# Kernel tuning notes

Hardware: AMD Instinct MI355X
Metric: run time of the kernel (lower is better)

The kernel has to match this reference:

```python
import jax, jax.numpy as jnp
import numpy as np

ROPE_BASE = 10000.0


def rotate_half(x):
    # interleaved rotate: (x0,x1,x2,x3,...) -> (-x1,x0,-x3,x2,...)
    x1 = x[..., ::2]
    x2 = x[..., 1::2]
    return jnp.stack((-x2, x1), axis=-1).reshape(x.shape)


def rope_cos_sin(seq_len, dim, dtype):
    inv_freq = 1.0 / (ROPE_BASE ** (jnp.arange(0, dim, 2, dtype=jnp.float32) / dim))
    pos = jnp.arange(seq_len, dtype=jnp.float32)
    freqs = jnp.outer(pos, inv_freq)              # [S, dim/2]
    emb = jnp.concatenate([freqs, freqs], axis=-1)  # [S, dim]
    return jnp.cos(emb).astype(dtype), jnp.sin(emb).astype(dtype)


def setup_inputs() -> dict:
    key = jax.random.key(0)
    k1, k2, k3, k4 = jax.random.split(key, 4)
    B, S, D = 4, 4096, 256
    scale = 1.0 / np.sqrt(D)
    x = jax.random.normal(k1, (B, S, D), dtype=jnp.float32)
    wq = jax.random.normal(k2, (D, D), dtype=jnp.float32) * scale
    wk = jax.random.normal(k3, (D, D), dtype=jnp.float32) * scale
    wv = jax.random.normal(k4, (D, D), dtype=jnp.float32) * scale
    return {"x": x, "wq": wq, "wk": wk, "wv": wv}


def reference(x, wq, wk, wv):
    D = x.shape[-1]
    S = x.shape[-2]
    # torch Linear: y = x @ W^T
    q = jnp.einsum('bsd,ed->bse', x, wq)
    k = jnp.einsum('bsd,ed->bse', x, wk)
    v = jnp.einsum('bsd,ed->bse', x, wv)
    cos, sin = rope_cos_sin(S, D, x.dtype)  # [S, D]
    q = q * cos + rotate_half(q) * sin
    k = k * cos + rotate_half(k) * sin
    scores = jnp.einsum('bqd,bkd->bqk', q, k) / jnp.sqrt(jnp.asarray(D, x.dtype))
    weights = jax.nn.softmax(scores, axis=-1)
    output = jnp.einsum('bqk,bkd->bqd', weights, v)
    return output, weights
```

## Files before the change

kernel.cpp:

```cpp
#include <hip/hip_runtime.h>
#include <hip/hip_bf16.h>
#include <stdint.h>


#define B_ 4
#define S_ 4096
#define D_ 256
#define NQ 4194304
#define NW 65536
#define NTAB 524288

typedef __attribute__((ext_vector_type(4))) float f32x4;
typedef __attribute__((ext_vector_type(8))) short short8;
typedef __attribute__((ext_vector_type(4))) short short4v;
typedef __attribute__((ext_vector_type(4))) unsigned uint32x4;

__device__ __forceinline__ short f2bf(float f) {
  unsigned u = __builtin_bit_cast(unsigned, f);
  u += 0x7fffu + ((u >> 16) & 1u);
  return (short)(u >> 16);
}
__device__ __forceinline__ float bf2f(short h) {
  unsigned u = ((unsigned)(unsigned short)h) << 16;
  return __builtin_bit_cast(float, u);
}

__device__ __forceinline__ void gload16(const void* g, void* l) {
  __builtin_amdgcn_global_load_lds(
      (const __attribute__((address_space(1))) unsigned*)g,
      (__attribute__((address_space(3))) unsigned*)l, 16, 0, 0);
}

__global__ __launch_bounds__(256) void k0_split(
    const float* __restrict__ wq, const float* __restrict__ wk,
    const float* __restrict__ wv,
    short* __restrict__ wh, short* __restrict__ wl,
    float* __restrict__ ctab) {
  int idx = blockIdx.x * 256 + threadIdx.x;
  if (idx < 3 * NW) {
    int m = idx >> 16;
    int e = idx & (NW - 1);
    const float* w = (m == 0) ? wq : (m == 1) ? wk : wv;
    float v = w[e];
    short hi = f2bf(v);
    wh[idx] = hi;
    wl[idx] = f2bf(v - bf2f(hi));
  } else {
    int t = idx - 3 * NW;
    int s = t >> 7, j = t & 127;
    float invf = __expf(-0.07195578415606394f * (float)j);
    float sn, cs;
    sincosf((float)s * invf, &sn, &cs);
    ctab[2 * t] = cs;
    ctab[2 * t + 1] = sn;
  }
}

__global__ __launch_bounds__(256) void k1_proj(
    const float* __restrict__ x,
    const short* __restrict__ wh, const short* __restrict__ wl,
    const float* __restrict__ ctab,
    short* __restrict__ qh, short* __restrict__ ql,
    short* __restrict__ kh, short* __restrict__ vt) {
  const int m = blockIdx.y;
  const int b = blockIdx.x >> 6;
  const int sbase = (blockIdx.x & 63) << 6;
  const int tid = threadIdx.x;
  const int w = tid >> 6;
  const int lane = tid & 63;
  const int lr = lane & 15;
  const int g = lane >> 4;

  const int srow = sbase + w * 16 + lr;
  const float* xp = x + ((size_t)(b * S_ + srow)) * D_;
  const short* whm = wh + m * NW;
  const short* wlm = wl + m * NW;

  short8 ah[8], al[8];
#pragma unroll
  for (int dc = 0; dc < 8; ++dc) {
    const float* xe = xp + dc * 32 + g * 8;
    f32x4 v0 = *(const f32x4*)(xe);
    f32x4 v1 = *(const f32x4*)(xe + 4);
#pragma unroll
    for (int j = 0; j < 4; ++j) {
      short h0 = f2bf(v0[j]);
      ah[dc][j] = h0;
      al[dc][j] = f2bf(v0[j] - bf2f(h0));
      short h1 = f2bf(v1[j]);
      ah[dc][4 + j] = h1;
      al[dc][4 + j] = f2bf(v1[j] - bf2f(h1));
    }
  }

  f32x4 acc[16];
#pragma unroll
  for (int i = 0; i < 16; ++i) acc[i] = (f32x4)0.f;

#pragma unroll
  for (int dc = 0; dc < 8; ++dc) {
    const int d = dc * 32 + g * 8;
#pragma unroll
    for (int ct = 0; ct < 16; ++ct) {
      const int e = ct * 16 + lr;
      short8 bh = *(const short8*)(whm + e * D_ + d);
      short8 bl = *(const short8*)(wlm + e * D_ + d);
      acc[ct] = __builtin_amdgcn_mfma_f32_16x16x32_bf16(ah[dc], bh, acc[ct], 0, 0, 0);
      acc[ct] = __builtin_amdgcn_mfma_f32_16x16x32_bf16(ah[dc], bl, acc[ct], 0, 0, 0);
      acc[ct] = __builtin_amdgcn_mfma_f32_16x16x32_bf16(al[dc], bh, acc[ct], 0, 0, 0);
    }
  }

  const int s0 = sbase + w * 16 + g * 4;
  if (m == 2) {
#pragma unroll
    for (int ct = 0; ct < 16; ++ct) {
      const int e = ct * 16 + lr;
      short4v pk;
#pragma unroll
      for (int r = 0; r < 4; ++r) pk[r] = f2bf(acc[ct][r]);
      *(short4v*)(vt + ((size_t)(b * D_ + e)) * S_ + s0) = pk;
    }
  } else {
    short* oh = (m == 0) ? qh : kh;
#pragma unroll
    for (int ct = 0; ct < 16; ++ct) {
      const int e = ct * 16 + lr;
      const float sgn = (e & 1) ? 1.0f : -1.0f;
#pragma unroll
      for (int r = 0; r < 4; ++r) {
        float v = acc[ct][r];
        float p = __shfl_xor(v, 1, 64);
        const float2 cs2 = *(const float2*)(ctab + ((size_t)((s0 + r) << 7) + (e & 127)) * 2);
        float q2 = v * cs2.x + sgn * p * cs2.y;
        short hi = f2bf(q2);
        size_t off = ((size_t)(b * S_ + s0 + r)) * D_ + e;
        oh[off] = hi;
        if (m == 0) ql[off] = f2bf(q2 - bf2f(hi));
      }
    }
  }
}

__global__ __launch_bounds__(256, 3) void k2_fused(
    const short* __restrict__ qh, const short* __restrict__ ql,
    const short* __restrict__ kh, const short* __restrict__ vt,
    float* __restrict__ wts, float* __restrict__ out) {
  __shared__ __align__(16) char kbuf[32768];
  __shared__ __align__(16) char etile[2][2048];
  __shared__ float part[2][32];
  __shared__ float lsum_l[32];

  const int bid = blockIdx.x;
  const int swz = (bid & 7) * 64 + ((bid >> 3) & 31) * 2 + (bid >> 8);
  const int b = swz >> 7;
  const int qbase = (swz & 127) << 5;
  const int tid = threadIdx.x;
  const int w = tid >> 6;
  const int lane = tid & 63;
  const int lr = lane & 15;
  const int g = lane >> 4;
  const int qg = w & 1;
  const int kg = w >> 1;

  short8 qfh[8], qfl[8];
  {
    const int qrow = qbase + qg * 16 + lr;
    const short* ph = qh + ((size_t)(b * S_ + qrow)) * D_;
    const short* pl = ql + ((size_t)(b * S_ + qrow)) * D_;
#pragma unroll
    for (int dc = 0; dc < 8; ++dc) {
      qfh[dc] = *(const short8*)(ph + dc * 32 + g * 8);
      qfl[dc] = *(const short8*)(pl + dc * 32 + g * 8);
    }
  }

  f32x4 acc = (f32x4)0.f;
  f32x4 accv[2][4];
#pragma unroll
  for (int qs = 0; qs < 2; ++qs)
#pragma unroll
    for (int dt = 0; dt < 4; ++dt) accv[qs][dt] = (f32x4)0.f;
  float rs = 0.f;

  const char* khb = (const char*)(kh + (size_t)b * S_ * D_);
  const short* vtb = vt + (size_t)b * D_ * S_;
  const int swx = (lane & 7) << 4;

  char* WB = (char*)(wts + ((size_t)(b * S_ + qbase)) * S_);
  char* EB = WB + 262144;

  auto STAGE = [&](int kt, char* dst) {
#pragma unroll
    for (int i = 0; i < 4; ++i) {
      const int p = i * 4096 + tid * 16;
      const int xo = p ^ (((p >> 9) & 7) << 4);
      gload16(khb + (size_t)kt * 16384 + xo, dst + p);
    }
  };

  STAGE(0, kbuf);
  __syncthreads();

  for (int kt = 0; kt < 128; ++kt) {
    const int cur = kt & 1;
    const char* kb = kbuf + cur * 16384;

    if (kt < 127) STAGE(kt + 1, kbuf + (cur ^ 1) * 16384);

    if (kt > 0) {
      const char* et = etile[cur ^ 1];
      {
        const int p = tid * 8;
        const int row = p >> 6, cb = p & 63;
        uint2 v = *(const uint2*)(et + (p ^ ((row & 3) << 4)));
        *(uint2*)(EB + (size_t)row * 8192 + (kt - 1) * 64 + cb) = v;
      }
      __builtin_amdgcn_s_setprio(1);
      short8 ea0 = *(const short8*)(et + ((lr * 64 + g * 16) ^ ((lr & 3) << 4)));
      short8 ea1 = *(const short8*)(et + (((16 + lr) * 64 + g * 16) ^ ((lr & 3) << 4)));
#pragma unroll
      for (int dt = 0; dt < 4; ++dt) {
        const int d = w * 64 + dt * 16 + lr;
        short8 vb = *(const short8*)(vtb + (size_t)d * S_ + (kt - 1) * 32 + g * 8);
        accv[0][dt] = __builtin_amdgcn_mfma_f32_16x16x32_bf16(ea0, vb, accv[0][dt], 0, 0, 0);
        accv[1][dt] = __builtin_amdgcn_mfma_f32_16x16x32_bf16(ea1, vb, accv[1][dt], 0, 0, 0);
      }
      __builtin_amdgcn_s_setprio(0);
    }

    __builtin_amdgcn_s_setprio(1);
#pragma unroll
    for (int dc = 0; dc < 8; ++dc) {
      const int row = kg * 16 + lr;
      const int x = (row * 512 + dc * 64 + g * 16) ^ swx;
      short8 afh = *(const short8*)(kb + x);
      acc = __builtin_amdgcn_mfma_f32_16x16x32_bf16(afh, qfh[dc], acc, 0, 0, 0);
      acc = __builtin_amdgcn_mfma_f32_16x16x32_bf16(afh, qfl[dc], acc, 0, 0, 0);
    }
    __builtin_amdgcn_s_setprio(0);

    {
      f32x4 e;
#pragma unroll
      for (int r = 0; r < 4; ++r) e[r] = __expf(acc[r] * 0.0625f);
      rs += e[0] + e[1] + e[2] + e[3];
      unsigned lo = (unsigned)(unsigned short)f2bf(e[0]) |
                    ((unsigned)(unsigned short)f2bf(e[1]) << 16);
      unsigned hi2 = (unsigned)(unsigned short)f2bf(e[2]) |
                     ((unsigned)(unsigned short)f2bf(e[3]) << 16);
      const int row = qg * 16 + lr;
      const int colb = (kg * 16 + g * 4) * 2;
      const int ad = (row * 64 + colb) ^ ((row & 3) << 4);
      *(uint2*)(etile[cur] + ad) = make_uint2(lo, hi2);
      acc = (f32x4)0.f;
    }
    __syncthreads();
  }

  {
    const char* et = etile[1];
    {
      const int p = tid * 8;
      const int row = p >> 6, cb = p & 63;
      uint2 v = *(const uint2*)(et + (p ^ ((row & 3) << 4)));
      *(uint2*)(EB + (size_t)row * 8192 + 127 * 64 + cb) = v;
    }
    short8 ea0 = *(const short8*)(et + ((lr * 64 + g * 16) ^ ((lr & 3) << 4)));
    short8 ea1 = *(const short8*)(et + (((16 + lr) * 64 + g * 16) ^ ((lr & 3) << 4)));
#pragma unroll
    for (int dt = 0; dt < 4; ++dt) {
      const int d = w * 64 + dt * 16 + lr;
      short8 vb = *(const short8*)(vtb + (size_t)d * S_ + 127 * 32 + g * 8);
      accv[0][dt] = __builtin_amdgcn_mfma_f32_16x16x32_bf16(ea0, vb, accv[0][dt], 0, 0, 0);
      accv[1][dt] = __builtin_amdgcn_mfma_f32_16x16x32_bf16(ea1, vb, accv[1][dt], 0, 0, 0);
    }
  }

  rs += __shfl_xor(rs, 16, 64);
  rs += __shfl_xor(rs, 32, 64);
  if (lane < 16) part[kg][qg * 16 + lane] = rs;
  __syncthreads();
  if (tid < 32) lsum_l[tid] = part[0][tid] + part[1][tid];
  __syncthreads();

#pragma unroll
  for (int i = 0; i < 4; ++i) {
    const int p = i * 4096 + tid * 16;
    *(uint32x4*)(kbuf + p) = *(const uint32x4*)(EB + (size_t)30 * 8192 + p);
  }

  {
    float* ob = out + (size_t)b * S_ * D_;
    float rv[2][4];
#pragma unroll
    for (int qs = 0; qs < 2; ++qs)
#pragma unroll
      for (int r = 0; r < 4; ++r)
        rv[qs][r] = 1.0f / lsum_l[qs * 16 + g * 4 + r];
#pragma unroll
    for (int qs = 0; qs < 2; ++qs)
#pragma unroll
      for (int dt = 0; dt < 4; ++dt)
#pragma unroll
        for (int r = 0; r < 4; ++r) {
          const int q = qbase + qs * 16 + g * 4 + r;
          ob[(size_t)q * D_ + w * 64 + dt * 16 + lr] = accv[qs][dt][r] * rv[qs][r];
        }
  }
  __syncthreads();

  const int pr0[5] = {0, 16, 24, 28, 30};
  const int pr1[5] = {16, 24, 28, 30, 32};
  float* WBf = (float*)WB;
#pragma unroll 1
  for (int ph = 0; ph < 5; ++ph) {
    for (int r = pr0[ph] + w; r < pr1[ph]; r += 4) {
      const float rinv = 1.0f / lsum_l[r];
      const short* erow = (r >= 30) ? (const short*)(kbuf + (size_t)(r - 30) * 8192)
                                    : (const short*)(EB + (size_t)r * 8192);
      float* wrow = WBf + (size_t)r * 4096;
      for (int c = lane * 8; c < 4096; c += 512) {
        short8 ev = *(const short8*)(erow + c);
        f32x4 o0, o1;
#pragma unroll
        for (int j = 0; j < 4; ++j) o0[j] = bf2f(ev[j]) * rinv;
#pragma unroll
        for (int j = 0; j < 4; ++j) o1[j] = bf2f(ev[4 + j]) * rinv;
        *(f32x4*)(wrow + c) = o0;
        *(f32x4*)(wrow + c + 4) = o1;
      }
    }
    __syncthreads();
  }
}

extern "C" void kernel_launch(void* const* d_in, const int* in_sizes, int n_in,
                              void* d_out, int out_size, void* d_ws, size_t ws_size,
                              hipStream_t stream) {
  const float* x  = (const float*)d_in[0];
  const float* wq = (const float*)d_in[1];
  const float* wk = (const float*)d_in[2];
  const float* wv = (const float*)d_in[3];

  float* out = (float*)d_out;
  float* wts = out + (size_t)B_ * S_ * D_;

  short* qh = (short*)d_ws;
  short* ql = qh + NQ;
  short* kh = ql + NQ;
  short* vt = kh + NQ;
  short* wh = vt + NQ;
  short* wl = wh + 3 * NW;
  float* ctab = (float*)(wl + 3 * NW);

  k0_split<<<dim3((3 * NW + NTAB) / 256), 256, 0, stream>>>(
      wq, wk, wv, wh, wl, ctab);
  k1_proj<<<dim3(B_ * S_ / 64, 3), 256, 0, stream>>>(
      x, wh, wl, ctab, qh, ql, kh, vt);
  k2_fused<<<dim3(512), 256, 0, stream>>>(
      qh, ql, kh, vt, wts, out);
}
```

Baseline: 427.2 us.

## Split fused attention into a bf16 exp-tile pass and a normalization pass

The fused attention kernel is split in two. The first pass computes unnormalized exp scores, stores them as bf16 in a workspace buffer, accumulates PV and the row sums, and writes the normalized output. A second lightweight kernel reads the bf16 exps and row sums and writes the normalized fp32 weights. This replaces the fused kernel's second pass over the weights with one streaming write, at the cost of 128MB of extra workspace traffic and an extra launch. It falls back to the fused kernel when the workspace is too small.

```diff
diff --git a/kernel.cpp b/kernel.cpp
--- a/kernel.cpp
+++ b/kernel.cpp
@@ -142,6 +142,199 @@
   }
 }
 
+
+__global__ __launch_bounds__(256, 3) void k2a(
+    const short* __restrict__ qh, const short* __restrict__ ql,
+    const short* __restrict__ kh, const short* __restrict__ vt,
+    char* __restrict__ ebg, float* __restrict__ lsum_g,
+    float* __restrict__ out) {
+  __shared__ __align__(16) char kbuf[32768];
+  __shared__ __align__(16) char etile[2][2048];
+  __shared__ float part[2][32];
+  __shared__ float lsum_l[32];
+
+  const int bid = blockIdx.x;
+  const int swz = (bid & 7) * 64 + ((bid >> 3) & 31) * 2 + (bid >> 8);
+  const int b = swz >> 7;
+  const int qbase = (swz & 127) << 5;
+  const int tid = threadIdx.x;
+  const int w = tid >> 6;
+  const int lane = tid & 63;
+  const int lr = lane & 15;
+  const int g = lane >> 4;
+  const int qg = w & 1;
+  const int kg = w >> 1;
+
+  short8 qfh[8], qfl[8];
+  {
+    const int qrow = qbase + qg * 16 + lr;
+    const short* ph = qh + ((size_t)(b * S_ + qrow)) * D_;
+    const short* pl = ql + ((size_t)(b * S_ + qrow)) * D_;
+#pragma unroll
+    for (int dc = 0; dc < 8; ++dc) {
+      qfh[dc] = *(const short8*)(ph + dc * 32 + g * 8);
+      qfl[dc] = *(const short8*)(pl + dc * 32 + g * 8);
+    }
+  }
+
+  f32x4 acc = (f32x4)0.f;
+  f32x4 accv[2][4];
+#pragma unroll
+  for (int qs = 0; qs < 2; ++qs)
+#pragma unroll
+    for (int dt = 0; dt < 4; ++dt) accv[qs][dt] = (f32x4)0.f;
+  float rs = 0.f;
+
+  const char* khb = (const char*)(kh + (size_t)b * S_ * D_);
+  const short* vtb = vt + (size_t)b * D_ * S_;
+  const int swx = (lane & 7) << 4;
+
+  char* EB = ebg + ((size_t)(b * S_ + qbase)) * 8192;
+
+  auto STAGE = [&](int kt, char* dst) {
+#pragma unroll
+    for (int i = 0; i < 4; ++i) {
+      const int p = i * 4096 + tid * 16;
+      const int xo = p ^ (((p >> 9) & 7) << 4);
+      gload16(khb + (size_t)kt * 16384 + xo, dst + p);
+    }
+  };
+
+  STAGE(0, kbuf);
+  __syncthreads();
+
+  for (int kt = 0; kt < 128; ++kt) {
+    const int cur = kt & 1;
+    const char* kb = kbuf + cur * 16384;
+
+    if (kt < 127) STAGE(kt + 1, kbuf + (cur ^ 1) * 16384);
+
+    if (kt > 0) {
+      const char* et = etile[cur ^ 1];
+      {
+        const int p = tid * 8;
+        const int row = p >> 6, cb = p & 63;
+        uint2 v = *(const uint2*)(et + (p ^ ((row & 3) << 4)));
+        *(uint2*)(EB + (size_t)row * 8192 + (kt - 1) * 64 + cb) = v;
+      }
+      __builtin_amdgcn_s_setprio(1);
+      short8 ea0 = *(const short8*)(et + ((lr * 64 + g * 16) ^ ((lr & 3) << 4)));
+      short8 ea1 = *(const short8*)(et + (((16 + lr) * 64 + g * 16) ^ ((lr & 3) << 4)));
+#pragma unroll
+      for (int dt = 0; dt < 4; ++dt) {
+        const int d = w * 64 + dt * 16 + lr;
+        short8 vb = *(const short8*)(vtb + (size_t)d * S_ + (kt - 1) * 32 + g * 8);
+        accv[0][dt] = __builtin_amdgcn_mfma_f32_16x16x32_bf16(ea0, vb, accv[0][dt], 0, 0, 0);
+        accv[1][dt] = __builtin_amdgcn_mfma_f32_16x16x32_bf16(ea1, vb, accv[1][dt], 0, 0, 0);
+      }
+      __builtin_amdgcn_s_setprio(0);
+    }
+
+    __builtin_amdgcn_s_setprio(1);
+#pragma unroll
+    for (int dc = 0; dc < 8; ++dc) {
+      const int row = kg * 16 + lr;
+      const int x = (row * 512 + dc * 64 + g * 16) ^ swx;
+      short8 afh = *(const short8*)(kb + x);
+      acc = __builtin_amdgcn_mfma_f32_16x16x32_bf16(afh, qfh[dc], acc, 0, 0, 0);
+      acc = __builtin_amdgcn_mfma_f32_16x16x32_bf16(afh, qfl[dc], acc, 0, 0, 0);
+    }
+    __builtin_amdgcn_s_setprio(0);
+
+    {
+      f32x4 e;
+#pragma unroll
+      for (int r = 0; r < 4; ++r) e[r] = __expf(acc[r] * 0.0625f);
+      rs += e[0] + e[1] + e[2] + e[3];
+      unsigned lo = (unsigned)(unsigned short)f2bf(e[0]) |
+                    ((unsigned)(unsigned short)f2bf(e[1]) << 16);
+      unsigned hi2 = (unsigned)(unsigned short)f2bf(e[2]) |
+                     ((unsigned)(unsigned short)f2bf(e[3]) << 16);
+      const int row = qg * 16 + lr;
+      const int colb = (kg * 16 + g * 4) * 2;
+      const int ad = (row * 64 + colb) ^ ((row & 3) << 4);
+      *(uint2*)(etile[cur] + ad) = make_uint2(lo, hi2);
+      acc = (f32x4)0.f;
+    }
+    __syncthreads();
+  }
+
+  {
+    const char* et = etile[1];
+    {
+      const int p = tid * 8;
+      const int row = p >> 6, cb = p & 63;
+      uint2 v = *(const uint2*)(et + (p ^ ((row & 3) << 4)));
+      *(uint2*)(EB + (size_t)row * 8192 + 127 * 64 + cb) = v;
+    }
+    short8 ea0 = *(const short8*)(et + ((lr * 64 + g * 16) ^ ((lr & 3) << 4)));
+    short8 ea1 = *(const short8*)(et + (((16 + lr) * 64 + g * 16) ^ ((lr & 3) << 4)));
+#pragma unroll
+    for (int dt = 0; dt < 4; ++dt) {
+      const int d = w * 64 + dt * 16 + lr;
+      short8 vb = *(const short8*)(vtb + (size_t)d * S_ + 127 * 32 + g * 8);
+      accv[0][dt] = __builtin_amdgcn_mfma_f32_16x16x32_bf16(ea0, vb, accv[0][dt], 0, 0, 0);
+      accv[1][dt] = __builtin_amdgcn_mfma_f32_16x16x32_bf16(ea1, vb, accv[1][dt], 0, 0, 0);
+    }
+  }
+
+  rs += __shfl_xor(rs, 16, 64);
+  rs += __shfl_xor(rs, 32, 64);
+  if (lane < 16) part[kg][qg * 16 + lane] = rs;
+  __syncthreads();
+  if (tid < 32) {
+    float l = part[0][tid] + part[1][tid];
+    lsum_l[tid] = l;
+    lsum_g[b * S_ + qbase + tid] = l;
+  }
+  __syncthreads();
+
+  {
+    float* ob = out + (size_t)b * S_ * D_;
+    float rv[2][4];
+#pragma unroll
+    for (int qs = 0; qs < 2; ++qs)
+#pragma unroll
+      for (int r = 0; r < 4; ++r)
+        rv[qs][r] = 1.0f / lsum_l[qs * 16 + g * 4 + r];
+#pragma unroll
+    for (int qs = 0; qs < 2; ++qs)
+#pragma unroll
+      for (int dt = 0; dt < 4; ++dt)
+#pragma unroll
+        for (int r = 0; r < 4; ++r) {
+          const int q = qbase + qs * 16 + g * 4 + r;
+          ob[(size_t)q * D_ + w * 64 + dt * 16 + lr] = accv[qs][dt][r] * rv[qs][r];
+        }
+  }
+}
+
+__global__ __launch_bounds__(256) void k2n(
+    const char* __restrict__ ebg, const float* __restrict__ lsum_g,
+    float* __restrict__ wts) {
+  const int tid = threadIdx.x;
+  for (int rr = 0; rr < 8; ++rr) {
+    const int row = blockIdx.x * 8 + rr;
+    const float rinv = 1.0f / lsum_g[row];
+    const short* er = (const short*)(ebg + (size_t)row * 8192) + tid * 16;
+    float* wr = wts + (size_t)row * 4096 + tid * 16;
+    short8 ev0 = *(const short8*)(er);
+    short8 ev1 = *(const short8*)(er + 8);
+    f32x4 o0, o1, o2, o3;
+#pragma unroll
+    for (int j = 0; j < 4; ++j) {
+      o0[j] = bf2f(ev0[j]) * rinv;
+      o1[j] = bf2f(ev0[4 + j]) * rinv;
+      o2[j] = bf2f(ev1[j]) * rinv;
+      o3[j] = bf2f(ev1[4 + j]) * rinv;
+    }
+    *(f32x4*)(wr) = o0;
+    *(f32x4*)(wr + 4) = o1;
+    *(f32x4*)(wr + 8) = o2;
+    *(f32x4*)(wr + 12) = o3;
+  }
+}
+
 __global__ __launch_bounds__(256, 3) void k2_fused(
     const short* __restrict__ qh, const short* __restrict__ ql,
     const short* __restrict__ kh, const short* __restrict__ vt,
@@ -353,11 +546,21 @@
   short* wh = vt + NQ;
   short* wl = wh + 3 * NW;
   float* ctab = (float*)(wl + 3 * NW);
+  char*  ebg  = (char*)(ctab + 2 * NTAB);
+  float* lsum_g = (float*)(ebg + (size_t)B_ * S_ * S_ * 2);
+
+  const size_t need_a = (size_t)(4 * NQ + 6 * NW) * 2 + (size_t)2 * NTAB * 4 +
+                        (size_t)B_ * S_ * S_ * 2 + (size_t)B_ * S_ * 4;
 
   k0_split<<<dim3((3 * NW + NTAB) / 256), 256, 0, stream>>>(
       wq, wk, wv, wh, wl, ctab);
   k1_proj<<<dim3(B_ * S_ / 64, 3), 256, 0, stream>>>(
       x, wh, wl, ctab, qh, ql, kh, vt);
-  k2_fused<<<dim3(512), 256, 0, stream>>>(
-      qh, ql, kh, vt, wts, out);
-}
+
+  if (ws_size >= need_a) {
+    k2a<<<dim3(512), 256, 0, stream>>>(qh, ql, kh, vt, ebg, lsum_g, out);
+    k2n<<<dim3(2048), 256, 0, stream>>>(ebg, lsum_g, wts);
+  } else {
+    k2_fused<<<dim3(512), 256, 0, stream>>>(qh, ql, kh, vt, wts, out);
+  }
+}
```

After: 467.3 us. 1.09x slower.

## Fuse Q/K/V projections into one block loop with half-column split per wave

Applied to the files above, without the earlier changes.

The projection kernel now loops over the Q, K and V weight matrices inside one block instead of using a separate grid dimension. Each x row tile is converted to hi/lo bf16 once and reused for all three projections, which removes the 3x reload and re-split of x. Each pair of waves shares 16 rows and splits the 256 output columns in half. This halves the accumulator registers and adds an occupancy hint. The cost is fewer blocks (512 instead of 768) and a sequential loop over the three matrices.

```diff
diff --git a/kernel.cpp b/kernel.cpp
--- a/kernel.cpp
+++ b/kernel.cpp
@@ -56,25 +56,25 @@
   }
 }
 
-__global__ __launch_bounds__(256) void k1_proj(
+__global__ __launch_bounds__(256, 2) void k1_proj(
     const float* __restrict__ x,
     const short* __restrict__ wh, const short* __restrict__ wl,
     const float* __restrict__ ctab,
     short* __restrict__ qh, short* __restrict__ ql,
     short* __restrict__ kh, short* __restrict__ vt) {
-  const int m = blockIdx.y;
-  const int b = blockIdx.x >> 6;
-  const int sbase = (blockIdx.x & 63) << 6;
+  const int bid = blockIdx.x;
+  const int b = bid >> 7;
+  const int sbase = (bid & 127) << 5;
   const int tid = threadIdx.x;
   const int w = tid >> 6;
   const int lane = tid & 63;
   const int lr = lane & 15;
   const int g = lane >> 4;
-
-  const int srow = sbase + w * 16 + lr;
+  const int qg2 = w >> 1;
+  const int ch = w & 1;
+
+  const int srow = sbase + qg2 * 16 + lr;
   const float* xp = x + ((size_t)(b * S_ + srow)) * D_;
-  const short* whm = wh + m * NW;
-  const short* wlm = wl + m * NW;
 
   short8 ah[8], al[8];
 #pragma unroll
@@ -93,50 +93,57 @@
     }
   }
 
-  f32x4 acc[16];
-#pragma unroll
-  for (int i = 0; i < 16; ++i) acc[i] = (f32x4)0.f;
-
-#pragma unroll
-  for (int dc = 0; dc < 8; ++dc) {
-    const int d = dc * 32 + g * 8;
-#pragma unroll
-    for (int ct = 0; ct < 16; ++ct) {
-      const int e = ct * 16 + lr;
-      short8 bh = *(const short8*)(whm + e * D_ + d);
-      short8 bl = *(const short8*)(wlm + e * D_ + d);
-      acc[ct] = __builtin_amdgcn_mfma_f32_16x16x32_bf16(ah[dc], bh, acc[ct], 0, 0, 0);
-      acc[ct] = __builtin_amdgcn_mfma_f32_16x16x32_bf16(ah[dc], bl, acc[ct], 0, 0, 0);
-      acc[ct] = __builtin_amdgcn_mfma_f32_16x16x32_bf16(al[dc], bh, acc[ct], 0, 0, 0);
-    }
-  }
-
-  const int s0 = sbase + w * 16 + g * 4;
-  if (m == 2) {
-#pragma unroll
-    for (int ct = 0; ct < 16; ++ct) {
-      const int e = ct * 16 + lr;
-      short4v pk;
-#pragma unroll
-      for (int r = 0; r < 4; ++r) pk[r] = f2bf(acc[ct][r]);
-      *(short4v*)(vt + ((size_t)(b * D_ + e)) * S_ + s0) = pk;
-    }
-  } else {
-    short* oh = (m == 0) ? qh : kh;
-#pragma unroll
-    for (int ct = 0; ct < 16; ++ct) {
-      const int e = ct * 16 + lr;
-      const float sgn = (e & 1) ? 1.0f : -1.0f;
-#pragma unroll
-      for (int r = 0; r < 4; ++r) {
-        float v = acc[ct][r];
-        float p = __shfl_xor(v, 1, 64);
-        const float2 cs2 = *(const float2*)(ctab + ((size_t)((s0 + r) << 7) + (e & 127)) * 2);
-        float q2 = v * cs2.x + sgn * p * cs2.y;
-        short hi = f2bf(q2);
-        size_t off = ((size_t)(b * S_ + s0 + r)) * D_ + e;
-        oh[off] = hi;
-        if (m == 0) ql[off] = f2bf(q2 - bf2f(hi));
+  const int s0 = sbase + qg2 * 16 + g * 4;
+
+#pragma unroll 1
+  for (int m = 0; m < 3; ++m) {
+    const short* whm = wh + m * NW;
+    const short* wlm = wl + m * NW;
+
+    f32x4 acc[8];
+#pragma unroll
+    for (int i = 0; i < 8; ++i) acc[i] = (f32x4)0.f;
+
+#pragma unroll
+    for (int dc = 0; dc < 8; ++dc) {
+      const int d = dc * 32 + g * 8;
+#pragma unroll
+      for (int c8 = 0; c8 < 8; ++c8) {
+        const int e = (ch * 8 + c8) * 16 + lr;
+        short8 bh = *(const short8*)(whm + e * D_ + d);
+        short8 bl = *(const short8*)(wlm + e * D_ + d);
+        acc[c8] = __builtin_amdgcn_mfma_f32_16x16x32_bf16(ah[dc], bh, acc[c8], 0, 0, 0);
+        acc[c8] = __builtin_amdgcn_mfma_f32_16x16x32_bf16(ah[dc], bl, acc[c8], 0, 0, 0);
+        acc[c8] = __builtin_amdgcn_mfma_f32_16x16x32_bf16(al[dc], bh, acc[c8], 0, 0, 0);
+      }
+    }
+
+    if (m == 2) {
+#pragma unroll
+      for (int c8 = 0; c8 < 8; ++c8) {
+        const int e = (ch * 8 + c8) * 16 + lr;
+        short4v pk;
+#pragma unroll
+        for (int r = 0; r < 4; ++r) pk[r] = f2bf(acc[c8][r]);
+        *(short4v*)(vt + ((size_t)(b * D_ + e)) * S_ + s0) = pk;
+      }
+    } else {
+      short* oh = (m == 0) ? qh : kh;
+#pragma unroll
+      for (int c8 = 0; c8 < 8; ++c8) {
+        const int e = (ch * 8 + c8) * 16 + lr;
+        const float sgn = (e & 1) ? 1.0f : -1.0f;
+#pragma unroll
+        for (int r = 0; r < 4; ++r) {
+          float v = acc[c8][r];
+          float p = __shfl_xor(v, 1, 64);
+          const float2 cs2 = *(const float2*)(ctab + ((size_t)((s0 + r) << 7) + (e & 127)) * 2);
+          float q2 = v * cs2.x + sgn * p * cs2.y;
+          short hi = f2bf(q2);
+          size_t off = ((size_t)(b * S_ + s0 + r)) * D_ + e;
+          oh[off] = hi;
+          if (m == 0) ql[off] = f2bf(q2 - bf2f(hi));
+        }
       }
     }
   }
@@ -356,7 +363,7 @@
 
   k0_split<<<dim3((3 * NW + NTAB) / 256), 256, 0, stream>>>(
       wq, wk, wv, wh, wl, ctab);
-  k1_proj<<<dim3(B_ * S_ / 64, 3), 256, 0, stream>>>(
+  k1_proj<<<dim3(B_ * S_ / 32), 256, 0, stream>>>(
       x, wh, wl, ctab, qh, ql, kh, vt);
   k2_fused<<<dim3(512), 256, 0, stream>>>(
       qh, ql, kh, vt, wts, out);
```

After: 392.3 us, median of 2. -8.2%, faster.
